# Kernel optimization log

Measured on AMD Instinct MI355X. Metric: run time of the kernel, lower is better.

Reference implementation:

```python
import jax, jax.numpy as jnp
import numpy as np

H = 16  # n_head

def setup_inputs() -> dict:
    key = jax.random.key(0)
    ks = jax.random.split(key, 6)
    d = 1024
    x = jax.random.normal(ks[0], (2, 2048, d), dtype=jnp.float32)
    s = 1.0 / np.sqrt(d)
    Wq = jax.random.normal(ks[1], (d, d), dtype=jnp.float32) * s
    Wk = jax.random.normal(ks[2], (d, d), dtype=jnp.float32) * s
    Wv = jax.random.normal(ks[3], (d, d), dtype=jnp.float32) * s
    Wo = jax.random.normal(ks[4], (d, d), dtype=jnp.float32) * s
    bo = jnp.zeros((d,), dtype=jnp.float32)
    return {"x": x, "Wq": Wq, "Wk": Wk, "Wv": Wv, "Wo": Wo, "bo": bo}

def reference(x, Wq, Wk, Wv, Wo, bo):
    b, n, dm = x.shape
    dh = dm // H
    scale = dh ** -0.5
    # projections (torch Linear: y = x @ W.T); weights stored as [out, in]
    q = (x @ Wq.T).reshape(b, n, H, dh).transpose(0, 2, 1, 3)  # b h n d
    k = (x @ Wk.T).reshape(b, n, H, dh).transpose(0, 2, 1, 3)
    v = (x @ Wv.T).reshape(b, n, H, dh).transpose(0, 2, 1, 3)
    sim = jnp.einsum('bhid,bhjd->bhij', q, k) * scale
    attn = jax.nn.softmax(sim, axis=-1)
    out = jnp.einsum('bhij,bhjd->bhid', attn, v)
    out = out.transpose(0, 2, 1, 3).reshape(b, n, dm)
    return out @ Wo.T + bo
```

## Files before the change

### kernel.cpp

```cpp
#include <hip/hip_runtime.h>
#include <hip/hip_bf16.h>
#include <cmath>

typedef unsigned short u16;
typedef __attribute__((ext_vector_type(8))) short short8;
typedef __attribute__((ext_vector_type(4))) float floatx4;
typedef __attribute__((ext_vector_type(4))) int intx4;
typedef __attribute__((ext_vector_type(2))) unsigned int uintx2;

#define NH     16
#define DHEAD  64
#define NSEQ   2048
#define DMODEL 1024
#define NBATCH 2
#define MTOT   (NBATCH * NSEQ)
#define XN     ((size_t)MTOT * DMODEL)
#define WN     ((size_t)DMODEL * DMODEL)

#define QSCALE 0.18033688011118545f

__device__ inline u16 f2bf(float f) {
    unsigned int u = __builtin_bit_cast(unsigned int, f);
    unsigned int rounding = 0x7FFFu + ((u >> 16) & 1u);
    return (u16)((u + rounding) >> 16);
}

__device__ inline unsigned int pkbf(float a, float b) {
    unsigned int ua = __builtin_bit_cast(unsigned int, a) + 0x8000u;
    unsigned int ub = __builtin_bit_cast(unsigned int, b) + 0x8000u;
    return __builtin_amdgcn_perm(ub, ua, 0x07060302u);
}

__device__ inline float fexp2(float x) {
#if __has_builtin(__builtin_amdgcn_exp2f)
    return __builtin_amdgcn_exp2f(x);
#else
    return exp2f(x);
#endif
}
__device__ inline float frcp(float x) {
#if __has_builtin(__builtin_amdgcn_rcpf)
    return __builtin_amdgcn_rcpf(x);
#else
    return 1.0f / x;
#endif
}

__device__ inline int jperm(int j) {
    return (j & 32) + ((j & 12) << 1) + ((j & 16) >> 2) + (j & 3);
}

__device__ inline short8 ld8(const float* p) {
    floatx4 a = *(const floatx4*)p;
    floatx4 b = *(const floatx4*)(p + 4);
    short8 r;
    r[0] = (short)f2bf(a[0]); r[1] = (short)f2bf(a[1]);
    r[2] = (short)f2bf(a[2]); r[3] = (short)f2bf(a[3]);
    r[4] = (short)f2bf(b[0]); r[5] = (short)f2bf(b[1]);
    r[6] = (short)f2bf(b[2]); r[7] = (short)f2bf(b[3]);
    return r;
}
__device__ inline short8 ld8(const u16* p) { return *(const short8*)p; }

__device__ inline void gl_lds16(const u16* g, short* l) {
    __builtin_amdgcn_global_load_lds(
        (const __attribute__((address_space(1))) unsigned int*)(const void*)g,
        (__attribute__((address_space(3))) unsigned int*)(void*)l, 16, 0, 0);
}

__global__ __launch_bounds__(256) void cvt_all(const float* __restrict__ x,
                                               const float* __restrict__ wq,
                                               const float* __restrict__ wk,
                                               const float* __restrict__ wv,
                                               const float* __restrict__ wo,
                                               u16* __restrict__ xb,
                                               u16* __restrict__ wqb,
                                               u16* __restrict__ wkb,
                                               u16* __restrict__ wvb,
                                               u16* __restrict__ wob)
{
    size_t t = (size_t)blockIdx.x * 256 + threadIdx.x;
    size_t e = t * 8;
    const float* s; u16* d; size_t off;
    if (e < XN) { s = x; d = xb; off = e; }
    else {
        size_t r = (e - XN) >> 20;
        off = (e - XN) & (WN - 1);
        s = (r == 0) ? wq : (r == 1) ? wk : (r == 2) ? wv : wo;
        d = (r == 0) ? wqb : (r == 1) ? wkb : (r == 2) ? wvb : wob;
    }
    *(short8*)&d[off] = ld8(&s[off]);
}

__global__ __launch_bounds__(256) void gemm_qkv(const u16* __restrict__ A,
                                                const u16* __restrict__ B0,
                                                const u16* __restrict__ B1,
                                                const u16* __restrict__ B2,
                                                u16* __restrict__ C0,
                                                u16* __restrict__ C1,
                                                u16* __restrict__ C2)
{
    __shared__ __align__(16) short As[128 * 64];
    __shared__ __align__(16) short Bs[128 * 64];

    const int tid  = threadIdx.x;
    const int w    = tid >> 6;
    const int lane = tid & 63;
    const int ln   = lane & 15;
    const int q    = lane >> 4;
    const int lx   = ln & 7;
    const int wm   = w >> 1;
    const int wn   = w & 1;
    const int m0   = blockIdx.y * 128;
    const int widx = blockIdx.x >> 3;
    const int col0 = (blockIdx.x & 7) * 128;
    const u16* Bp  = (widx == 0 ? B0 : (widx == 1 ? B1 : B2));

    const int rsub = lane >> 3;
    const int kcl  = (lane & 7) ^ (rsub & 7);

    floatx4 acc[4][4];
#pragma unroll
    for (int i = 0; i < 4; ++i)
#pragma unroll
        for (int j = 0; j < 4; ++j) acc[i][j] = (floatx4){0.f, 0.f, 0.f, 0.f};

    for (int k0 = 0; k0 < DMODEL; k0 += 64) {
#pragma unroll
        for (int i = 0; i < 4; ++i) {
            const int r = (w * 4 + i) * 8 + rsub;
            gl_lds16(&A [(size_t)(m0 + r)   * DMODEL + k0 + kcl * 8], &As[(w * 4 + i) * 512]);
            gl_lds16(&Bp[(size_t)(col0 + r) * DMODEL + k0 + kcl * 8], &Bs[(w * 4 + i) * 512]);
        }
        __syncthreads();
#pragma unroll
        for (int kk = 0; kk < 2; ++kk) {
            short8 af[4], bf[4];
#pragma unroll
            for (int t = 0; t < 4; ++t) {
                af[t] = *(short8*)&As[(wm * 64 + t * 16 + ln) * 64 + (((kk * 4 + q) ^ lx) * 8)];
                bf[t] = *(short8*)&Bs[(wn * 64 + t * 16 + ln) * 64 + (((kk * 4 + q) ^ lx) * 8)];
            }
            if (widx != 2) {
#pragma unroll
                for (int mt = 0; mt < 4; ++mt)
#pragma unroll
                    for (int nt = 0; nt < 4; ++nt)
                        acc[mt][nt] = __builtin_amdgcn_mfma_f32_16x16x32_bf16(af[mt], bf[nt], acc[mt][nt], 0, 0, 0);
            } else {
#pragma unroll
                for (int mt = 0; mt < 4; ++mt)
#pragma unroll
                    for (int nt = 0; nt < 4; ++nt)
                        acc[mt][nt] = __builtin_amdgcn_mfma_f32_16x16x32_bf16(bf[mt], af[nt], acc[mt][nt], 0, 0, 0);
            }
        }
        __syncthreads();
    }

    if (widx != 2) {
        u16* Cw = (widx == 0 ? C0 : C1);
        const float oscale = (widx == 0) ? QSCALE : 1.0f;
#pragma unroll
        for (int mt = 0; mt < 4; ++mt) {
#pragma unroll
            for (int nt = 0; nt < 4; ++nt) {
                const int coln = wn * 64 + nt * 16 + ln;
#pragma unroll
                for (int reg = 0; reg < 4; ++reg) {
                    const int grow = m0 + wm * 64 + mt * 16 + q * 4 + reg;
                    const float v = acc[mt][nt][reg] * oscale;
                    const int gcol = col0 + coln;
                    const int h = gcol >> 6, d = gcol & 63;
                    const int b = grow >> 11, tok = grow & 2047;
                    Cw[((size_t)(b * NH + h) * NSEQ + tok) * DHEAD + d] = f2bf(v);
                }
            }
        }
    } else {
#pragma unroll
        for (int mt = 0; mt < 4; ++mt) {
#pragma unroll
            for (int nt = 0; nt < 4; ++nt) {
                const int tokg = m0 + wm * 64 + nt * 16 + ln;
                const int b = tokg >> 11, tok = tokg & 2047;
                const int tokp = (tok & ~63) + jperm(tok & 63);
#pragma unroll
                for (int reg = 0; reg < 4; ++reg) {
                    const int gcol = col0 + wn * 64 + mt * 16 + q * 4 + reg;
                    const int h = gcol >> 6, d = gcol & 63;
                    C2[((size_t)(b * NH + h) * DHEAD + d) * NSEQ + tokp] = f2bf(acc[mt][nt][reg]);
                }
            }
        }
    }
}

__global__ __launch_bounds__(256) void gemm_op(const u16* __restrict__ A,
                                               const u16* __restrict__ B,
                                               const float* __restrict__ bias,
                                               float* __restrict__ C)
{
    __shared__ __align__(16) short As[64 * 64];
    __shared__ __align__(16) short Bs[128 * 64];

    const int tid  = threadIdx.x;
    const int w    = tid >> 6;
    const int lane = tid & 63;
    const int ln   = lane & 15;
    const int q    = lane >> 4;
    const int lx   = ln & 7;
    const int wm   = w >> 1;
    const int wn   = w & 1;
    const int m0   = blockIdx.y * 64;
    const int n0   = blockIdx.x * 128;

    const int rsub = lane >> 3;
    const int kcl  = (lane & 7) ^ (rsub & 7);

    floatx4 acc[2][4];
#pragma unroll
    for (int i = 0; i < 2; ++i)
#pragma unroll
        for (int j = 0; j < 4; ++j) acc[i][j] = (floatx4){0.f, 0.f, 0.f, 0.f};

    for (int k0 = 0; k0 < DMODEL; k0 += 64) {
#pragma unroll
        for (int i = 0; i < 2; ++i) {
            const int c = w * 2 + i;
            gl_lds16(&A[(size_t)(m0 + c * 8 + rsub) * DMODEL + k0 + kcl * 8], &As[c * 512]);
        }
#pragma unroll
        for (int i = 0; i < 4; ++i) {
            const int c = w * 4 + i;
            gl_lds16(&B[(size_t)(n0 + c * 8 + rsub) * DMODEL + k0 + kcl * 8], &Bs[c * 512]);
        }
        __syncthreads();
#pragma unroll
        for (int kk = 0; kk < 2; ++kk) {
            short8 af[2], bf[4];
#pragma unroll
            for (int t = 0; t < 2; ++t)
                af[t] = *(short8*)&As[(wm * 32 + t * 16 + ln) * 64 + (((kk * 4 + q) ^ lx) * 8)];
#pragma unroll
            for (int t = 0; t < 4; ++t)
                bf[t] = *(short8*)&Bs[(wn * 64 + t * 16 + ln) * 64 + (((kk * 4 + q) ^ lx) * 8)];
#pragma unroll
            for (int mt = 0; mt < 2; ++mt)
#pragma unroll
                for (int nt = 0; nt < 4; ++nt)
                    acc[mt][nt] = __builtin_amdgcn_mfma_f32_16x16x32_bf16(af[mt], bf[nt], acc[mt][nt], 0, 0, 0);
        }
        __syncthreads();
    }

#pragma unroll
    for (int mt = 0; mt < 2; ++mt) {
#pragma unroll
        for (int nt = 0; nt < 4; ++nt) {
            const int coln = wn * 64 + nt * 16 + ln;
            const float bval = bias[n0 + coln];
#pragma unroll
            for (int reg = 0; reg < 4; ++reg) {
                const int grow = m0 + wm * 32 + mt * 16 + q * 4 + reg;
                C[(size_t)grow * DMODEL + n0 + coln] = acc[mt][nt][reg] + bval;
            }
        }
    }
}

__global__ __launch_bounds__(256) void attn6(const u16* __restrict__ Q,
                                             const u16* __restrict__ K,
                                             const u16* __restrict__ Vt,
                                             u16* __restrict__ O)
{
    __shared__ __align__(16) short Kb[2][64 * 64];
    __shared__ __align__(16) short Vb[2][64 * 64];

    const int tid  = threadIdx.x;
    const int w    = tid >> 6;
    const int lane = tid & 63;
    const int ln   = lane & 15;
    const int q    = lane >> 4;
    const int lx   = ln & 7;
    const int bid  = blockIdx.x;
    const int bh   = bid & 31;
    const int qt   = bid >> 5;
    const int row0 = qt * 128 + w * 32;
    const size_t sbase = (size_t)bh * NSEQ;
    const size_t vbase = (size_t)bh * DHEAD;

    const int rsub = lane >> 3;
    const int swz  = (lane & 7) ^ (rsub & 7);

    const intx4 onesi = {0x3F803F80, 0x3F803F80, 0x3F803F80, 0x3F803F80};
    const short8 ones = __builtin_bit_cast(short8, onesi);

    short8 bq[2][2];
#pragma unroll
    for (int mt = 0; mt < 2; ++mt)
#pragma unroll
        for (int kk = 0; kk < 2; ++kk)
            bq[mt][kk] = *(const short8*)&Q[(sbase + row0 + mt * 16 + ln) * DHEAD + kk * 32 + q * 8];

    floatx4 zero = {0.f, 0.f, 0.f, 0.f};
    floatx4 o[2][4];
    floatx4 ol[2];
#pragma unroll
    for (int mt = 0; mt < 2; ++mt) {
        ol[mt] = zero;
#pragma unroll
        for (int dt = 0; dt < 4; ++dt) o[mt][dt] = zero;
    }

#pragma unroll
    for (int i = 0; i < 2; ++i) {
        const int c = w * 2 + i;
        const int row = c * 8 + rsub;
        gl_lds16(&K [(sbase + row) * DHEAD + swz * 8], &Kb[0][c * 512]);
        gl_lds16(&Vt[(vbase + row) * NSEQ + swz * 8],  &Vb[0][c * 512]);
    }

    for (int kt = 0; kt < NSEQ / 64; ++kt) {
        __syncthreads();
        const int cur = kt & 1;
        if (kt + 1 < NSEQ / 64) {
            const int kb = (kt + 1) * 64;
#pragma unroll
            for (int i = 0; i < 2; ++i) {
                const int c = w * 2 + i;
                const int row = c * 8 + rsub;
                gl_lds16(&K [(sbase + kb + row) * DHEAD + swz * 8], &Kb[cur ^ 1][c * 512]);
                gl_lds16(&Vt[(vbase + row) * NSEQ + kb + swz * 8],  &Vb[cur ^ 1][c * 512]);
            }
        }

        floatx4 st[4][2];
#pragma unroll
        for (int t = 0; t < 4; ++t) {
            short8 ak0 = *(short8*)&Kb[cur][(t * 16 + ln) * 64 + ((q ^ lx) * 8)];
            short8 ak1 = *(short8*)&Kb[cur][(t * 16 + ln) * 64 + (((4 + q) ^ lx) * 8)];
#pragma unroll
            for (int mt = 0; mt < 2; ++mt) {
                st[t][mt] = zero;
                st[t][mt] = __builtin_amdgcn_mfma_f32_16x16x32_bf16(ak0, bq[mt][0], st[t][mt], 0, 0, 0);
                st[t][mt] = __builtin_amdgcn_mfma_f32_16x16x32_bf16(ak1, bq[mt][1], st[t][mt], 0, 0, 0);
            }
        }

        intx4 bp[2][2];
#pragma unroll
        for (int mt = 0; mt < 2; ++mt) {
#pragma unroll
            for (int t = 0; t < 4; ++t) {
                floatx4 p;
#pragma unroll
                for (int r = 0; r < 4; ++r) p[r] = fexp2(st[t][mt][r]);
                bp[t >> 1][mt][(t & 1) * 2 + 0] = (int)pkbf(p[0], p[1]);
                bp[t >> 1][mt][(t & 1) * 2 + 1] = (int)pkbf(p[2], p[3]);
            }
        }

#pragma unroll
        for (int mt = 0; mt < 2; ++mt)
#pragma unroll
            for (int c = 0; c < 2; ++c)
                ol[mt] = __builtin_amdgcn_mfma_f32_16x16x32_bf16(
                    ones, __builtin_bit_cast(short8, bp[c][mt]), ol[mt], 0, 0, 0);

#pragma unroll
        for (int dt = 0; dt < 4; ++dt) {
#pragma unroll
            for (int c = 0; c < 2; ++c) {
                short8 av = *(short8*)&Vb[cur][(dt * 16 + ln) * 64 + (((4 * c + q) ^ lx) * 8)];
#pragma unroll
                for (int mt = 0; mt < 2; ++mt)
                    o[mt][dt] = __builtin_amdgcn_mfma_f32_16x16x32_bf16(
                        av, __builtin_bit_cast(short8, bp[c][mt]), o[mt][dt], 0, 0, 0);
            }
        }
    }

    float l[2];
#pragma unroll
    for (int mt = 0; mt < 2; ++mt) l[mt] = frcp(ol[mt][0]);

    const int b = bh >> 4, h = bh & 15;
#pragma unroll
    for (int mt = 0; mt < 2; ++mt) {
        const int tok = row0 + mt * 16 + ln;
#pragma unroll
        for (int dt = 0; dt < 4; ++dt) {
            uintx2 pk;
            pk[0] = pkbf(o[mt][dt][0] * l[mt], o[mt][dt][1] * l[mt]);
            pk[1] = pkbf(o[mt][dt][2] * l[mt], o[mt][dt][3] * l[mt]);
            *(uintx2*)&O[((size_t)(b * NSEQ + tok)) * DMODEL + h * DHEAD + dt * 16 + q * 4] = pk;
        }
    }
}

template <int MODE, typename TA, typename TB>
__global__ __launch_bounds__(256) void gemm_bt(const TA* __restrict__ A,
                                               const TB* __restrict__ B,
                                               const float* __restrict__ bias,
                                               void* __restrict__ Cv,
                                               float oscale)
{
    __shared__ __align__(16) short As[64][72];
    __shared__ __align__(16) short Bs[64][72];

    const int tid  = threadIdx.x;
    const int w    = tid >> 6;
    const int lane = tid & 63;
    const int ln   = lane & 15;
    const int q    = lane >> 4;
    const int wm   = w >> 1;
    const int wn   = w & 1;
    const int m0   = blockIdx.y * 64;
    const int n0   = blockIdx.x * 64;
    const int r    = tid >> 3;
    const int c8   = (tid & 7) * 8;

    floatx4 zero = {0.f, 0.f, 0.f, 0.f};
    floatx4 acc[2][2];
    acc[0][0] = zero; acc[0][1] = zero; acc[1][0] = zero; acc[1][1] = zero;

    for (int k0 = 0; k0 < DMODEL; k0 += 64) {
        *(short8*)&As[r][c8]      = ld8(&A[(size_t)(m0 + r) * DMODEL + k0 + c8]);
        *(short8*)&As[r + 32][c8] = ld8(&A[(size_t)(m0 + r + 32) * DMODEL + k0 + c8]);
        *(short8*)&Bs[r][c8]      = ld8(&B[(size_t)(n0 + r) * DMODEL + k0 + c8]);
        *(short8*)&Bs[r + 32][c8] = ld8(&B[(size_t)(n0 + r + 32) * DMODEL + k0 + c8]);
        __syncthreads();
#pragma unroll
        for (int kk = 0; kk < 2; ++kk) {
            short8 a0 = *(short8*)&As[wm * 32 + ln][kk * 32 + q * 8];
            short8 a1 = *(short8*)&As[wm * 32 + 16 + ln][kk * 32 + q * 8];
            short8 b0 = *(short8*)&Bs[wn * 32 + ln][kk * 32 + q * 8];
            short8 b1 = *(short8*)&Bs[wn * 32 + 16 + ln][kk * 32 + q * 8];
            acc[0][0] = __builtin_amdgcn_mfma_f32_16x16x32_bf16(a0, b0, acc[0][0], 0, 0, 0);
            acc[0][1] = __builtin_amdgcn_mfma_f32_16x16x32_bf16(a0, b1, acc[0][1], 0, 0, 0);
            acc[1][0] = __builtin_amdgcn_mfma_f32_16x16x32_bf16(a1, b0, acc[1][0], 0, 0, 0);
            acc[1][1] = __builtin_amdgcn_mfma_f32_16x16x32_bf16(a1, b1, acc[1][1], 0, 0, 0);
        }
        __syncthreads();
    }

#pragma unroll
    for (int mt = 0; mt < 2; ++mt) {
#pragma unroll
        for (int nt = 0; nt < 2; ++nt) {
            const int coln = wn * 32 + nt * 16 + ln;
            float bval = 0.f;
            if (MODE == 0) bval = bias[n0 + coln];
#pragma unroll
            for (int reg = 0; reg < 4; ++reg) {
                const int grow = m0 + wm * 32 + mt * 16 + q * 4 + reg;
                const float v = acc[mt][nt][reg] * oscale + bval;
                if (MODE == 0) {
                    ((float*)Cv)[(size_t)grow * DMODEL + n0 + coln] = v;
                } else {
                    const int b = grow >> 11, tok = grow & 2047, h = n0 >> 6;
                    if (MODE == 1)
                        ((u16*)Cv)[((size_t)(b * NH + h) * NSEQ + tok) * DHEAD + coln] = f2bf(v);
                    else {
                        const int tokp = (tok & ~63) + jperm(tok & 63);
                        ((u16*)Cv)[((size_t)(b * NH + h) * DHEAD + coln) * NSEQ + tokp] = f2bf(v);
                    }
                }
            }
        }
    }
}

extern "C" void kernel_launch(void* const* d_in, const int* in_sizes, int n_in,
                              void* d_out, int out_size, void* d_ws, size_t ws_size,
                              hipStream_t stream) {
    (void)in_sizes; (void)n_in; (void)out_size;
    const float* x  = (const float*)d_in[0];
    const float* Wq = (const float*)d_in[1];
    const float* Wk = (const float*)d_in[2];
    const float* Wv = (const float*)d_in[3];
    const float* Wo = (const float*)d_in[4];
    const float* bo = (const float*)d_in[5];
    float* out = (float*)d_out;

    dim3 bb(256);
    dim3 ga(512);

    const size_t NEED = XN * 2 + 4 * WN * 2 + 3 * XN * 2;
    if (ws_size >= NEED) {
        u16* xb  = (u16*)d_ws;
        u16* Wqb = xb + XN;
        u16* Wkb = Wqb + WN;
        u16* Wvb = Wkb + WN;
        u16* Wob = Wvb + WN;
        u16* Qb  = Wob + WN;
        u16* Kb  = Qb + XN;
        u16* Vtb = Kb + XN;
        u16* Ob  = xb;

        cvt_all<<<dim3((unsigned)((XN + 4 * WN) / 8 / 256)), bb, 0, stream>>>(
            x, Wq, Wk, Wv, Wo, xb, Wqb, Wkb, Wvb, Wob);

        gemm_qkv<<<dim3(24, 32), bb, 0, stream>>>(xb, Wqb, Wkb, Wvb, Qb, Kb, Vtb);
        attn6<<<ga, bb, 0, stream>>>(Qb, Kb, Vtb, Ob);
        gemm_op<<<dim3(8, 64), bb, 0, stream>>>(Ob, Wob, bo, out);
    } else {
        u16* Qb  = (u16*)d_ws;
        u16* Kb  = Qb + XN;
        u16* Vtb = Kb + XN;
        u16* Ob  = Vtb + XN;
        dim3 gg(DMODEL / 64, MTOT / 64);
        gemm_bt<1, float, float><<<gg, bb, 0, stream>>>(x, Wq, nullptr, Qb, QSCALE);
        gemm_bt<1, float, float><<<gg, bb, 0, stream>>>(x, Wk, nullptr, Kb, 1.0f);
        gemm_bt<2, float, float><<<gg, bb, 0, stream>>>(x, Wv, nullptr, Vtb, 1.0f);
        attn6<<<ga, bb, 0, stream>>>(Qb, Kb, Vtb, Ob);
        gemm_bt<0, u16, float><<<gg, bb, 0, stream>>>(Ob, Wo, bo, out, 1.0f);
    }
}
```

Baseline: 183.8 us.

## Split key sequence across two wave groups per attention block and merge via LDS

The attention kernel now launches 512 threads per block, with two groups of four waves each processing half of the key/value sequence for the same query tile. Each group has its own double-buffered K/V staging in LDS. At the end, the partial outputs and row sums are combined through shared memory before the bf16 output is written. This shortens the serial key loop per wave and raises the number of resident waves to hide latency, at the cost of doubled LDS use and an extra reduction step.

```diff
diff --git a/kernel.cpp b/kernel.cpp
--- a/kernel.cpp
+++ b/kernel.cpp
@@ -269,16 +269,18 @@
     }
 }
 
-__global__ __launch_bounds__(256) void attn6(const u16* __restrict__ Q,
+__global__ __launch_bounds__(512) void attn7(const u16* __restrict__ Q,
                                              const u16* __restrict__ K,
                                              const u16* __restrict__ Vt,
                                              u16* __restrict__ O)
 {
-    __shared__ __align__(16) short Kb[2][64 * 64];
-    __shared__ __align__(16) short Vb[2][64 * 64];
+    __shared__ __align__(16) short Kb[2][2][64 * 64];
+    __shared__ __align__(16) short Vb[2][2][64 * 64];
 
     const int tid  = threadIdx.x;
     const int w    = tid >> 6;
+    const int g    = w >> 2;
+    const int wl   = w & 3;
     const int lane = tid & 63;
     const int ln   = lane & 15;
     const int q    = lane >> 4;
@@ -286,9 +288,10 @@
     const int bid  = blockIdx.x;
     const int bh   = bid & 31;
     const int qt   = bid >> 5;
-    const int row0 = qt * 128 + w * 32;
+    const int row0 = qt * 128 + wl * 32;
     const size_t sbase = (size_t)bh * NSEQ;
     const size_t vbase = (size_t)bh * DHEAD;
+    const int kt0 = g * 16;
 
     const int rsub = lane >> 3;
     const int swz  = (lane & 7) ^ (rsub & 7);
@@ -315,31 +318,31 @@
 
 #pragma unroll
     for (int i = 0; i < 2; ++i) {
-        const int c = w * 2 + i;
+        const int c = wl * 2 + i;
         const int row = c * 8 + rsub;
-        gl_lds16(&K [(sbase + row) * DHEAD + swz * 8], &Kb[0][c * 512]);
-        gl_lds16(&Vt[(vbase + row) * NSEQ + swz * 8],  &Vb[0][c * 512]);
-    }
-
-    for (int kt = 0; kt < NSEQ / 64; ++kt) {
-        __syncthreads();
-        const int cur = kt & 1;
-        if (kt + 1 < NSEQ / 64) {
-            const int kb = (kt + 1) * 64;
+        gl_lds16(&K [(sbase + kt0 * 64 + row) * DHEAD + swz * 8], &Kb[g][0][c * 512]);
+        gl_lds16(&Vt[(vbase + row) * NSEQ + kt0 * 64 + swz * 8],  &Vb[g][0][c * 512]);
+    }
+
+    for (int it = 0; it < 16; ++it) {
+        __syncthreads();
+        const int cur = it & 1;
+        if (it + 1 < 16) {
+            const int kb = (kt0 + it + 1) * 64;
 #pragma unroll
             for (int i = 0; i < 2; ++i) {
-                const int c = w * 2 + i;
+                const int c = wl * 2 + i;
                 const int row = c * 8 + rsub;
-                gl_lds16(&K [(sbase + kb + row) * DHEAD + swz * 8], &Kb[cur ^ 1][c * 512]);
-                gl_lds16(&Vt[(vbase + row) * NSEQ + kb + swz * 8],  &Vb[cur ^ 1][c * 512]);
+                gl_lds16(&K [(sbase + kb + row) * DHEAD + swz * 8], &Kb[g][cur ^ 1][c * 512]);
+                gl_lds16(&Vt[(vbase + row) * NSEQ + kb + swz * 8],  &Vb[g][cur ^ 1][c * 512]);
             }
         }
 
         floatx4 st[4][2];
 #pragma unroll
         for (int t = 0; t < 4; ++t) {
-            short8 ak0 = *(short8*)&Kb[cur][(t * 16 + ln) * 64 + ((q ^ lx) * 8)];
-            short8 ak1 = *(short8*)&Kb[cur][(t * 16 + ln) * 64 + (((4 + q) ^ lx) * 8)];
+            short8 ak0 = *(short8*)&Kb[g][cur][(t * 16 + ln) * 64 + ((q ^ lx) * 8)];
+            short8 ak1 = *(short8*)&Kb[g][cur][(t * 16 + ln) * 64 + (((4 + q) ^ lx) * 8)];
 #pragma unroll
             for (int mt = 0; mt < 2; ++mt) {
                 st[t][mt] = zero;
@@ -372,7 +375,7 @@
         for (int dt = 0; dt < 4; ++dt) {
 #pragma unroll
             for (int c = 0; c < 2; ++c) {
-                short8 av = *(short8*)&Vb[cur][(dt * 16 + ln) * 64 + (((4 * c + q) ^ lx) * 8)];
+                short8 av = *(short8*)&Vb[g][cur][(dt * 16 + ln) * 64 + (((4 * c + q) ^ lx) * 8)];
 #pragma unroll
                 for (int mt = 0; mt < 2; ++mt)
                     o[mt][dt] = __builtin_amdgcn_mfma_f32_16x16x32_bf16(
@@ -381,20 +384,36 @@
         }
     }
 
-    float l[2];
-#pragma unroll
-    for (int mt = 0; mt < 2; ++mt) l[mt] = frcp(ol[mt][0]);
-
-    const int b = bh >> 4, h = bh & 15;
-#pragma unroll
-    for (int mt = 0; mt < 2; ++mt) {
-        const int tok = row0 + mt * 16 + ln;
-#pragma unroll
-        for (int dt = 0; dt < 4; ++dt) {
-            uintx2 pk;
-            pk[0] = pkbf(o[mt][dt][0] * l[mt], o[mt][dt][1] * l[mt]);
-            pk[1] = pkbf(o[mt][dt][2] * l[mt], o[mt][dt][3] * l[mt]);
-            *(uintx2*)&O[((size_t)(b * NSEQ + tok)) * DMODEL + h * DHEAD + dt * 16 + q * 4] = pk;
+    __syncthreads();
+    float* of = (float*)&Kb[0][0][0];
+    float* lf = (float*)&Vb[1][1][0];
+    if (g == 1) {
+#pragma unroll
+        for (int mt = 0; mt < 2; ++mt) {
+#pragma unroll
+            for (int dt = 0; dt < 4; ++dt)
+                *(floatx4*)&of[(wl * 32 + mt * 16 + ln) * 68 + dt * 16 + q * 4] = o[mt][dt];
+            lf[wl * 32 + mt * 16 + ln] = ol[mt][0];
+        }
+    }
+    __syncthreads();
+    if (g == 0) {
+        const int b = bh >> 4, h = bh & 15;
+        float l[2];
+#pragma unroll
+        for (int mt = 0; mt < 2; ++mt)
+            l[mt] = frcp(ol[mt][0] + lf[wl * 32 + mt * 16 + ln]);
+#pragma unroll
+        for (int mt = 0; mt < 2; ++mt) {
+            const int tok = row0 + mt * 16 + ln;
+#pragma unroll
+            for (int dt = 0; dt < 4; ++dt) {
+                floatx4 p = *(floatx4*)&of[(wl * 32 + mt * 16 + ln) * 68 + dt * 16 + q * 4];
+                uintx2 pk;
+                pk[0] = pkbf((o[mt][dt][0] + p[0]) * l[mt], (o[mt][dt][1] + p[1]) * l[mt]);
+                pk[1] = pkbf((o[mt][dt][2] + p[2]) * l[mt], (o[mt][dt][3] + p[3]) * l[mt]);
+                *(uintx2*)&O[((size_t)(b * NSEQ + tok)) * DMODEL + h * DHEAD + dt * 16 + q * 4] = pk;
+            }
         }
     }
 }
@@ -485,6 +504,7 @@
     float* out = (float*)d_out;
 
     dim3 bb(256);
+    dim3 ba(512);
     dim3 ga(512);
 
     const size_t NEED = XN * 2 + 4 * WN * 2 + 3 * XN * 2;
@@ -503,7 +523,7 @@
             x, Wq, Wk, Wv, Wo, xb, Wqb, Wkb, Wvb, Wob);
 
         gemm_qkv<<<dim3(24, 32), bb, 0, stream>>>(xb, Wqb, Wkb, Wvb, Qb, Kb, Vtb);
-        attn6<<<ga, bb, 0, stream>>>(Qb, Kb, Vtb, Ob);
+        attn7<<<ga, ba, 0, stream>>>(Qb, Kb, Vtb, Ob);
         gemm_op<<<dim3(8, 64), bb, 0, stream>>>(Ob, Wob, bo, out);
     } else {
         u16* Qb  = (u16*)d_ws;
@@ -514,7 +534,7 @@
         gemm_bt<1, float, float><<<gg, bb, 0, stream>>>(x, Wq, nullptr, Qb, QSCALE);
         gemm_bt<1, float, float><<<gg, bb, 0, stream>>>(x, Wk, nullptr, Kb, 1.0f);
         gemm_bt<2, float, float><<<gg, bb, 0, stream>>>(x, Wv, nullptr, Vtb, 1.0f);
-        attn6<<<ga, bb, 0, stream>>>(Qb, Kb, Vtb, Ob);
+        attn7<<<ga, ba, 0, stream>>>(Qb, Kb, Vtb, Ob);
         gemm_bt<0, u16, float><<<gg, bb, 0, stream>>>(Ob, Wo, bo, out, 1.0f);
     }
 }
```

Result: no change. 181.1 us (-1.5%).
